# Optimization experiments

Hardware: AMD Instinct MI355X
Metric: run time of the kernel (lower is better)

Reference implementation:

```python
import jax, jax.numpy as jnp
import numpy as np

SCORE_THRESHOLD = 0.3
IOU_THRESHOLD = 0.5
TOP_K = 200
MAX_NMS_SIZE = 100
NEG = jnp.float32(-1e30)
NEG_HALF = jnp.float32(-1e29)


def _nms_per_class(scores, boxes):
    """Exact greedy NMS for one class. scores [N], boxes [N,4] (y1,x1,y2,x2).
    Returns (sel_scores [M], sel_boxes [M,4], valids [M]) with M=MAX_NMS_SIZE,
    zero-padded where fewer than M boxes survive (matches tf pad behavior)."""
    N = scores.shape[0]
    areas = jnp.prod(boxes[:, 2:] - boxes[:, :2], axis=-1)  # [N]
    arange_n = jnp.arange(N)
    # tf.image.non_max_suppression drops boxes with score < score_threshold
    masked0 = jnp.where(scores > SCORE_THRESHOLD, scores, NEG)

    def step(masked, _):
        idx = jnp.argmax(masked)
        s = masked[idx]
        valid = s > NEG_HALF
        box = boxes[idx]
        # IoU of selected box vs all boxes
        yx1 = jnp.maximum(box[:2], boxes[:, :2])
        yx2 = jnp.minimum(box[2:], boxes[:, 2:])
        inter = jnp.prod(jnp.maximum(yx2 - yx1, 0.0), axis=-1)
        union = jnp.prod(box[2:] - box[:2]) + areas - inter
        iou = jnp.where(union > 0, inter / union, 0.0)
        suppress = (iou > IOU_THRESHOLD) | (arange_n == idx)
        masked = jnp.where(valid & suppress, NEG, masked)
        return masked, (idx, valid, jnp.where(valid, s, 0.0))

    _, (idxs, valids, sel_scores) = jax.lax.scan(step, masked0, None, length=MAX_NMS_SIZE)
    sel_boxes = jnp.where(valids[:, None], boxes[idxs], 0.0)
    return sel_scores, sel_boxes, valids


def _per_sample(scores, boxes):
    """scores [N,C], boxes [N,4] -> (top_k_scores [K,2], top_k_boxes [K,4])."""
    cls_scores = scores[:, 1:].T  # [C-1, N]; class 0 (background) skipped
    sel_scores, sel_boxes, valids = jax.vmap(_nms_per_class, in_axes=(0, None))(cls_scores, boxes)
    ncls = cls_scores.shape[0]
    class_ids = jnp.where(valids, jnp.arange(1, ncls + 1, dtype=jnp.float32)[:, None], 0.0)
    flat_scores = jnp.stack([class_ids, sel_scores], axis=-1).reshape(-1, 2)  # [(C-1)*M, 2]
    flat_boxes = sel_boxes.reshape(-1, 4)
    n = flat_scores.shape[0]
    if TOP_K > n:  # static shapes -> Python-level pad branch
        flat_scores = jnp.pad(flat_scores, ((0, TOP_K - n), (0, 0)))
        flat_boxes = jnp.pad(flat_boxes, ((0, TOP_K - n), (0, 0)))
    _, top_idx = jax.lax.top_k(flat_scores[:, 1], TOP_K)
    return flat_scores[top_idx], flat_boxes[top_idx]


def setup_inputs() -> dict:
    key = jax.random.key(0)
    k1, k2, k3 = jax.random.split(key, 3)
    B, N, C = 16, 16384, 91
    scores_pred = jax.random.uniform(k1, (B, N, C), dtype=jnp.float32)
    tl = jax.random.uniform(k2, (B, N, 2), dtype=jnp.float32) * 0.8
    wh = jax.random.uniform(k3, (B, N, 2), dtype=jnp.float32) * 0.2 + 0.01
    boxes_pred = jnp.concatenate([tl, tl + wh], axis=-1)  # valid corner boxes
    return {"scores_pred": scores_pred, "boxes_pred": boxes_pred}


@jax.jit
def reference(scores_pred, boxes_pred):
    return jax.vmap(_per_sample)(scores_pred, boxes_pred)
```

## Files before the change

kernel.cpp:

```cpp
#include <hip/hip_runtime.h>

#define NTH 256
#define NBOX 16384
#define NCLSIN 91
#define NCLS 90
#define MAXSEL 100
#define TOPK 200
#define TSEL 256
#define CAP 1024
#define CANDL 512
#define CBCAP 256
#define BINS 1024
#define GRP 4
#define T0 0.989f
#define BOXPB 256
#define KSL 16
#define OVFC 64
#define CNTSTR 16

__device__ __forceinline__ unsigned fmap(float f) {
    unsigned u = __float_as_uint(f);
    return (u & 0x80000000u) ? ~u : (u | 0x80000000u);
}
__device__ __forceinline__ float funmap(unsigned u) {
    unsigned b = (u & 0x80000000u) ? (u ^ 0x80000000u) : ~u;
    return __uint_as_float(b);
}
__device__ __forceinline__ unsigned long long shfl_xor_u64(unsigned long long v, int mask) {
    unsigned lo = (unsigned)(v & 0xFFFFFFFFull);
    unsigned hi = (unsigned)(v >> 32);
    lo = __shfl_xor(lo, mask, 64);
    hi = __shfl_xor(hi, mask, 64);
    return ((unsigned long long)hi << 32) | (unsigned long long)lo;
}

__device__ __forceinline__ bool sup_test(float4 s, float sa, float4 c, float ca) {
    float y1 = fmaxf(s.x, c.x);
    float x1 = fmaxf(s.y, c.y);
    float y2 = fminf(s.z, c.z);
    float x2 = fminf(s.w, c.w);
    float dy = fmaxf(__fsub_rn(y2, y1), 0.f);
    float dx = fmaxf(__fsub_rn(x2, x1), 0.f);
    float inter = __fmul_rn(dy, dx);
    float uni = __fsub_rn(__fadd_rn(sa, ca), inter);
    if (!(uni > 0.f)) return false;
    float t = 0.5f * uni;
    if (inter <= t) return false;
    if (inter > __fmul_rn(t, 1.0000005f)) return true;
    return __fdiv_rn(inter, uni) > 0.5f;
}
__device__ __forceinline__ float box_area(float4 b) {
    return __fmul_rn(__fsub_rn(b.z, b.x), __fsub_rn(b.w, b.y));
}

__global__ __launch_bounds__(NTH) void zero_k(int4* __restrict__ p, int n4) {
    int i = blockIdx.x * NTH + threadIdx.x;
    if (i < n4) p[i] = make_int4(0, 0, 0, 0);
}

__device__ __forceinline__ void bin_select(unsigned* hist, unsigned* gbuf,
                                           int* sh_g, int* sh_b, unsigned* sh_pb,
                                           int tid, unsigned need) {
    unsigned gs = 0;
#pragma unroll
    for (int q = 0; q < GRP; ++q) gs += hist[tid * GRP + q];
    gbuf[tid] = gs;
    __syncthreads();
    for (int off = 1; off < NTH; off <<= 1) {
        unsigned add = (tid >= off) ? gbuf[tid - off] : 0u;
        __syncthreads();
        gbuf[tid] += add;
        __syncthreads();
    }
    if (tid == 0) *sh_g = NTH - 1;
    __syncthreads();
    if (gbuf[tid] >= need && (tid == 0 || gbuf[tid - 1] < need)) *sh_g = tid;
    __syncthreads();
    if (tid == 0) {
        int g = *sh_g;
        unsigned acc = (g > 0) ? gbuf[g - 1] : 0u;
        int bs = g * GRP + (GRP - 1);
        unsigned pb = acc;
#pragma unroll
        for (int q = 0; q < GRP; ++q) {
            acc += hist[g * GRP + q];
            if (acc >= need) { bs = g * GRP + q; pb = acc; break; }
            pb = acc;
        }
        *sh_b = bs; *sh_pb = pb;
    }
    __syncthreads();
}

__device__ __forceinline__ void sort_desc(unsigned long long* cand, int M, int tid) {
    int P = 1;
    while (P < M) P <<= 1;
    for (int i = M + tid; i < P; i += NTH) cand[i] = 0ull;
    __syncthreads();
    for (int kk = 2; kk <= P; kk <<= 1) {
        for (int jj = kk >> 1; jj > 0; jj >>= 1) {
            for (int i = tid; i < P; i += NTH) {
                int ixj = i ^ jj;
                if (ixj > i) {
                    unsigned long long a = cand[i], c = cand[ixj];
                    bool sw = ((i & kk) == 0) ? (a < c) : (a > c);
                    if (sw) { cand[i] = c; cand[ixj] = a; }
                }
            }
            __syncthreads();
        }
    }
}

__device__ __forceinline__ void emit_hit(unsigned long long pk, int b, int n0,
                                         int* cnt_s, unsigned long long* ent,
                                         unsigned* ovf_meta,
                                         unsigned long long* ovf_key,
                                         int* sh_ovf, int* cnt_g) {
    unsigned ee = (unsigned)pk;
    int row = (int)ee / NCLSIN;
    int c = (int)ee - row * NCLSIN;
    if (c == 0) return;
    unsigned i = (unsigned)(n0 + row);
    unsigned long long key = (pk & 0xFFFFFFFF00000000ull) | (0xFFFFFFFFu - i);
    int r = atomicAdd(&cnt_s[c], 1);
    if (r < KSL) {
        ent[c * KSL + r] = key;
    } else {
        int o = atomicAdd(sh_ovf, 1);
        if (o < OVFC) {
            ovf_meta[o] = ((unsigned)c << 16) | (unsigned)r;
            ovf_key[o] = key;
        } else {
            atomicAdd(&cnt_g[(b * NCLS + c - 1) * CNTSTR], CAP + 1);
        }
    }
}

__global__ __launch_bounds__(NTH) void filter_k(const float* __restrict__ in,
                                                unsigned long long* __restrict__ cand_g,
                                                int* __restrict__ cnt_g) {
    __shared__ int cnt_s[NCLSIN];
    __shared__ int base_s[NCLSIN];
    __shared__ unsigned long long ent[NCLSIN * KSL];
    __shared__ unsigned ovf_meta[OVFC];
    __shared__ unsigned long long ovf_key[OVFC];
    __shared__ int sh_ovf;

    const int tid = threadIdx.x;
    const int n0 = blockIdx.x * BOXPB;
    const int b = blockIdx.y;
    const int NF4 = BOXPB * NCLSIN / 4;

    for (int i = tid; i < NCLSIN; i += NTH) cnt_s[i] = 0;
    if (tid == 0) sh_ovf = 0;
    __syncthreads();

    unsigned long long q0 = 0, q1 = 0, q2 = 0, q3 = 0;
    int lc = 0;

    const float4* src = (const float4*)(in + ((size_t)b * NBOX + n0) * NCLSIN);
    for (int i = tid; i < NF4; i += 2 * NTH) {
        float4 v1 = src[i];
        int i2 = i + NTH;
        bool has2 = i2 < NF4;
        float4 v2 = make_float4(0.f, 0.f, 0.f, 0.f);
        if (has2) v2 = src[i2];
        float mx1 = fmaxf(fmaxf(v1.x, v1.y), fmaxf(v1.z, v1.w));
        float mx2 = fmaxf(fmaxf(v2.x, v2.y), fmaxf(v2.z, v2.w));
        if (fmaxf(mx1, mx2) > T0) {
#pragma unroll
            for (int h = 0; h < 2; ++h) {
                float4 v = h ? v2 : v1;
                float mx = h ? mx2 : mx1;
                int eb = (h ? i2 : i) * 4;
                if (mx > T0) {
                    const float sv[4] = {v.x, v.y, v.z, v.w};
#pragma unroll
                    for (int qq = 0; qq < 4; ++qq) {
                        float s = sv[qq];
                        if (s > T0) {
                            unsigned long long pk =
                                ((unsigned long long)fmap(s) << 32) |
                                (unsigned)(eb + qq);
                            if (lc == 0) q0 = pk;
                            else if (lc == 1) q1 = pk;
                            else if (lc == 2) q2 = pk;
                            else if (lc == 3) q3 = pk;
                            else emit_hit(pk, b, n0, cnt_s, ent, ovf_meta,
                                          ovf_key, &sh_ovf, cnt_g);
                            ++lc;
                        }
                    }
                }
            }
        }
    }
    if (lc > 0) emit_hit(q0, b, n0, cnt_s, ent, ovf_meta, ovf_key, &sh_ovf, cnt_g);
    if (lc > 1) emit_hit(q1, b, n0, cnt_s, ent, ovf_meta, ovf_key, &sh_ovf, cnt_g);
    if (lc > 2) emit_hit(q2, b, n0, cnt_s, ent, ovf_meta, ovf_key, &sh_ovf, cnt_g);
    if (lc > 3) emit_hit(q3, b, n0, cnt_s, ent, ovf_meta, ovf_key, &sh_ovf, cnt_g);
    __syncthreads();

    if (tid >= 1 && tid < NCLSIN) {
        int c = tid;
        int n = cnt_s[c];
        int base = 0;
        if (n > 0) {
            int bc = b * NCLS + c - 1;
            base = atomicAdd(&cnt_g[bc * CNTSTR], n);
            int lim = n < KSL ? n : KSL;
            for (int j = 0; j < lim; ++j) {
                int pos = base + j;
                if (pos < CAP) cand_g[(size_t)bc * CAP + pos] = ent[c * KSL + j];
            }
        }
        base_s[c] = base;
    }
    __syncthreads();

    int no = sh_ovf < OVFC ? sh_ovf : OVFC;
    for (int o = tid; o < no; o += NTH) {
        unsigned m = ovf_meta[o];
        int c = (int)(m >> 16);
        int r = (int)(m & 0xFFFFu);
        int bc = b * NCLS + c - 1;
        int pos = base_s[c] + r;
        if (pos < CAP) cand_g[(size_t)bc * CAP + pos] = ovf_key[o];
    }
}

__device__ __forceinline__ void serial_walk_lds(
    const unsigned long long* cand, int from, int to,
    const float4* __restrict__ bbase, const float4* candbox, const float* carea,
    float4* selbox, float* selarea, float* selscore,
    int& nsel, int* sh_nsel, int tid) {
    if (tid < 64) {
        for (int m = from; m < to && nsel < MAXSEL; ++m) {
            unsigned long long key = cand[m];
            float4 bx;
            float ca;
            if (m < CBCAP) { bx = candbox[m]; ca = carea[m]; }
            else { bx = bbase[(int)(0xFFFFFFFFu - (unsigned)key)]; ca = box_area(bx); }
            bool sup = false;
            if (tid < nsel) sup = sup_test(selbox[tid], selarea[tid], bx, ca);
            int l2 = tid + 64;
            if (l2 < nsel) sup = sup || sup_test(selbox[l2], selarea[l2], bx, ca);
            if (!__any(sup)) {
                if (tid == 0) {
                    selbox[nsel] = bx;
                    selarea[nsel] = ca;
                    selscore[nsel] = funmap((unsigned)(key >> 32));
                }
                nsel++;
            }
        }
        if (tid == 0) *sh_nsel = nsel;
    }
    __syncthreads();
    nsel = *sh_nsel;
    __syncthreads();
}

__global__ __launch_bounds__(NTH) void nms_k(
    const unsigned long long* __restrict__ cand_g,
    const int* __restrict__ cnt_g,
    const float* __restrict__ scores_raw,
    const float4* __restrict__ boxes,
    float* __restrict__ ws_sc, float* __restrict__ ws_bx, int use_band) {
    __shared__ unsigned long long cand[CANDL];
    __shared__ float4 candbox[CBCAP];
    __shared__ float carea[CBCAP];
    __shared__ float4 selbox[MAXSEL];
    __shared__ float selarea[MAXSEL];
    __shared__ float selscore[MAXSEL];
    __shared__ unsigned M32[CBCAP * 2];
    __shared__ unsigned gbuf[NTH];
    __shared__ unsigned sh_kmax, sh_pb;
    __shared__ int sh_E, sh_g, sh_b, sh_cnt, sh_nsel;
    unsigned* hist = (unsigned*)candbox;

    const int tid = threadIdx.x;
    const int c0 = blockIdx.x;
    const int b = blockIdx.y;
    const int bc = b * NCLS + c0;
    const float* sraw = scores_raw + (size_t)b * NBOX * NCLSIN + (c0 + 1);
    const float4* bbase = boxes + (size_t)b * NBOX;

    int nsel = 0;
    unsigned long long lastk = ~0ull;

    if (use_band) {
        const int C = cnt_g[bc * CNTSTR];
        if (C > 0 && C <= CANDL) {
            if (C <= 256) {
                unsigned long long v =
                    (tid < C) ? cand_g[(size_t)bc * CAP + tid] : 0ull;
#pragma unroll
                for (int kk = 2; kk <= 256; kk <<= 1) {
#pragma unroll
                    for (int jj = kk >> 1; jj > 0; jj >>= 1) {
                        unsigned long long o;
                        if (jj >= 64) {
                            cand[tid] = v;
                            __syncthreads();
                            o = cand[tid ^ jj];
                            __syncthreads();
                        } else {
                            o = shfl_xor_u64(v, jj);
                        }
                        bool lower = (tid & jj) == 0;
                        bool desc = (tid & kk) == 0;
                        v = (lower == desc) ? (v > o ? v : o) : (v < o ? v : o);
                    }
                }
                cand[tid] = v;
                __syncthreads();

                if (tid < C) {
                    float4 bx = bbase[(int)(0xFFFFFFFFu - (unsigned)cand[tid])];
                    candbox[tid] = bx;
                    carea[tid] = box_area(bx);
                }
                M32[tid] = 0;
                M32[tid + NTH] = 0;
                __syncthreads();

                const int nbatch = (C + 63) >> 6;
                for (int p = tid; p < nbatch * 2016; p += NTH) {
                    int bt = p / 2016;
                    int q = p - bt * 2016;
                    int i = (int)((1.0f + sqrtf(1.0f + 8.0f * (float)q)) * 0.5f);
                    while (i * (i - 1) / 2 > q) --i;
                    while ((i + 1) * i / 2 <= q) ++i;
                    int j = q - i * (i - 1) / 2;
                    int gm = bt * 64 + i, gj = bt * 64 + j;
                    if (gm < C) {
                        if (sup_test(candbox[gj], carea[gj], candbox[gm], carea[gm]))
                            atomicOr(&M32[gm * 2 + (j >> 5)], 1u << (j & 31));
                    }
                }
                __syncthreads();

                if (tid < 64) {
                    for (int bt = 0; bt < nbatch && nsel < MAXSEL; ++bt) {
                        int m = bt * 64 + tid;
                        bool active = m < C;
                        float4 bx = make_float4(0.f, 0.f, 0.f, 0.f);
                        float ca = 0.f;
                        unsigned long long key = 0ull;
                        unsigned long long myM = 0ull;
                        if (active) {
                            key = cand[m];
                            bx = candbox[m];
                            ca = carea[m];
                            myM = ((unsigned long long)M32[m * 2 + 1] << 32) |
                                  M32[m * 2];
                        }
                        bool supV = !active;
                        for (int j = 0; j < nsel; ++j) {
                            if (active)
                                supV = supV || sup_test(selbox[j], selarea[j], bx, ca);
                        }
                        unsigned long long selb = ~__ballot(supV);
                        unsigned long long U = __ballot(myM != 0ull) & selb;
                        while (U) {
                            int mm = __builtin_ctzll(U);
                            U &= U - 1ull;
                            unsigned long long Mm =
                                ((unsigned long long)M32[(bt * 64 + mm) * 2 + 1] << 32) |
                                M32[(bt * 64 + mm) * 2];
                            unsigned long long below =
                                (mm == 0) ? 0ull : ((1ull << mm) - 1ull);
                            if ((selb >> mm) & 1ull) {
                                if (Mm & selb & below) selb &= ~(1ull << mm);
                            }
                        }
                        int avail = MAXSEL - nsel;
                        int pop = __builtin_popcountll(selb);
                        while (pop > avail) {
                            selb &= ~(1ull << (63 - __builtin_clzll(selb)));
                            --pop;
                        }
                        if ((selb >> tid) & 1ull) {
                            unsigned long long below =
                                (tid == 0) ? 0ull : ((1ull << tid) - 1ull);
                            int pos = nsel + __builtin_popcountll(selb & below);
                            selbox[pos] = bx;
                            selarea[pos] = ca;
                            selscore[pos] = funmap((unsigned)(key >> 32));
                        }
                        nsel += pop;
                    }
                    if (tid == 0) sh_nsel = nsel;
                }
                __syncthreads();
                nsel = sh_nsel;
                __syncthreads();
            } else {
                for (int i = tid; i < C; i += NTH)
                    cand[i] = cand_g[(size_t)bc * CAP + i];
                sort_desc(cand, C, tid);
                const int PBX = C < CBCAP ? C : CBCAP;
                for (int i = tid; i < PBX; i += NTH) {
                    float4 bx = bbase[(int)(0xFFFFFFFFu - (unsigned)cand[i])];
                    candbox[i] = bx;
                    carea[i] = box_area(bx);
                }
                __syncthreads();
                serial_walk_lds(cand, 0, C, bbase, candbox, carea,
                                selbox, selarea, selscore, nsel, &sh_nsel, tid);
            }
            lastk = cand[C - 1];
        }
    }

    while (nsel < MAXSEL) {
        unsigned km = 0, ce = 0;
        for (int i = tid; i < NBOX; i += NTH) {
            float s = sraw[(size_t)i * NCLSIN];
            unsigned k = (s > 0.3f) ? fmap(s) : 0u;
            if (k) {
                unsigned long long key =
                    ((unsigned long long)k << 32) | (0xFFFFFFFFu - (unsigned)i);
                if (key < lastk) { ce++; km = km > k ? km : k; }
            }
        }
#pragma unroll
        for (int off = 32; off > 0; off >>= 1) {
            unsigned o = (unsigned)__shfl_xor((int)km, off, 64);
            km = km > o ? km : o;
            ce += (unsigned)__shfl_xor((int)ce, off, 64);
        }
        if ((tid & 63) == 0) { gbuf[tid >> 6] = km; gbuf[8 + (tid >> 6)] = ce; }
        __syncthreads();
        if (tid == 0) {
            unsigned m2 = 0, c2 = 0;
            for (int w = 0; w < NTH / 64; ++w) {
                m2 = m2 > gbuf[w] ? m2 : gbuf[w];
                c2 += gbuf[8 + w];
            }
            sh_kmax = m2; sh_E = (int)c2;
        }
        __syncthreads();
        const int E = sh_E;
        const unsigned kmax = sh_kmax;
        if (E == 0) break;

        unsigned thr = 1u;
        if (E > TSEL) {
            for (int shift = 8;; shift += 4) {
                for (int i = tid; i < BINS; i += NTH) hist[i] = 0u;
                __syncthreads();
                for (int i = tid; i < NBOX; i += NTH) {
                    float s = sraw[(size_t)i * NCLSIN];
                    unsigned k = (s > 0.3f) ? fmap(s) : 0u;
                    if (k) {
                        unsigned long long key =
                            ((unsigned long long)k << 32) | (0xFFFFFFFFu - (unsigned)i);
                        if (key < lastk) {
                            unsigned bin = (kmax - k) >> shift;
                            if (bin < BINS - 1) atomicAdd(&hist[bin], 1u);
                        }
                    }
                }
                __syncthreads();
                bin_select(hist, gbuf, &sh_g, &sh_b, &sh_pb, tid, (unsigned)TSEL);
                if (sh_b < BINS - 1) {
                    long long t = (long long)kmax - ((long long)(sh_b + 1) << shift) + 1;
                    thr = (t < 1) ? 1u : (unsigned)t;
                    break;
                }
            }
        }

        if (tid == 0) sh_cnt = 0;
        __syncthreads();
        for (int i = tid; i < NBOX; i += NTH) {
            float s = sraw[(size_t)i * NCLSIN];
            unsigned k = (s > 0.3f) ? fmap(s) : 0u;
            if (k >= thr) {
                unsigned long long key =
                    ((unsigned long long)k << 32) | (0xFFFFFFFFu - (unsigned)i);
                if (key < lastk) {
                    int pos = atomicAdd(&sh_cnt, 1);
                    if (pos < CANDL) cand[pos] = key;
                }
            }
        }
        __syncthreads();
        const int M = sh_cnt < CANDL ? sh_cnt : CANDL;

        sort_desc(cand, M, tid);
        const int PBX = M < CBCAP ? M : CBCAP;
        for (int i = tid; i < PBX; i += NTH) {
            float4 bx = bbase[(int)(0xFFFFFFFFu - (unsigned)cand[i])];
            candbox[i] = bx;
            carea[i] = box_area(bx);
        }
        __syncthreads();
        serial_walk_lds(cand, 0, M, bbase, candbox, carea,
                        selbox, selarea, selscore, nsel, &sh_nsel, tid);
        if (nsel >= MAXSEL || E <= M) break;
        lastk = cand[M - 1];
        __syncthreads();
    }

    if (tid < MAXSEL) {
        bool v = tid < nsel;
        ws_sc[(size_t)bc * MAXSEL + tid] = v ? selscore[tid] : 0.f;
        ((float4*)ws_bx)[(size_t)bc * MAXSEL + tid] =
            v ? selbox[tid] : make_float4(0.f, 0.f, 0.f, 0.f);
    }
}

__global__ __launch_bounds__(NTH) void topk_k(const float* __restrict__ ws_sc,
                                              const float* __restrict__ ws_bx,
                                              float* __restrict__ out_sc,
                                              float* __restrict__ out_bx) {
    __shared__ unsigned hist[BINS];
    __shared__ unsigned gbuf[NTH];
    __shared__ unsigned long long cand[CANDL];
    __shared__ unsigned sh_kmax, sh_pb;
    __shared__ int sh_E, sh_g, sh_b, sh_cnt;

    const int tid = threadIdx.x;
    const int b = blockIdx.x;
    const int NF = NCLS * MAXSEL;
    const float* sp = ws_sc + (size_t)b * NF;

    unsigned km = 0, ce = 0;
    for (int f = tid; f < NF; f += NTH) {
        unsigned k = __float_as_uint(sp[f]);
        if (k) { ce++; km = km > k ? km : k; }
    }
#pragma unroll
    for (int off = 32; off > 0; off >>= 1) {
        unsigned o = (unsigned)__shfl_xor((int)km, off, 64);
        km = km > o ? km : o;
        ce += (unsigned)__shfl_xor((int)ce, off, 64);
    }
    if ((tid & 63) == 0) { gbuf[tid >> 6] = km; gbuf[8 + (tid >> 6)] = ce; }
    __syncthreads();
    if (tid == 0) {
        unsigned m2 = 0, c2 = 0;
        for (int w = 0; w < NTH / 64; ++w) {
            m2 = m2 > gbuf[w] ? m2 : gbuf[w];
            c2 += gbuf[8 + w];
        }
        sh_kmax = m2; sh_E = (int)c2;
    }
    __syncthreads();
    const int E = sh_E;
    const unsigned kmax = sh_kmax;

    unsigned thr = 1u;
    if (E > TOPK) {
        for (int shift = 8;; shift += 4) {
            for (int i = tid; i < BINS; i += NTH) hist[i] = 0u;
            __syncthreads();
            for (int f = tid; f < NF; f += NTH) {
                unsigned k = __float_as_uint(sp[f]);
                if (k) {
                    unsigned bin = (kmax - k) >> shift;
                    if (bin < BINS - 1) atomicAdd(&hist[bin], 1u);
                }
            }
            __syncthreads();
            bin_select(hist, gbuf, &sh_g, &sh_b, &sh_pb, tid, (unsigned)TOPK);
            if (sh_b < BINS - 1) {
                long long t = (long long)kmax - ((long long)(sh_b + 1) << shift) + 1;
                thr = (t < 1) ? 1u : (unsigned)t;
                break;
            }
        }
    }

    if (tid == 0) sh_cnt = 0;
    __syncthreads();
    for (int f = tid; f < NF; f += NTH) {
        unsigned k = __float_as_uint(sp[f]);
        if (k >= thr) {
            int pos = atomicAdd(&sh_cnt, 1);
            if (pos < CANDL)
                cand[pos] = ((unsigned long long)k << 32) | (0xFFFFFFFFu - (unsigned)f);
        }
    }
    __syncthreads();
    int M = sh_cnt < CANDL ? sh_cnt : CANDL;

    if (M < TOPK) {
        int lim = M + TOPK;
        if (lim > NF) lim = NF;
        for (int f = tid; f < lim; f += NTH) {
            unsigned k = __float_as_uint(sp[f]);
            if (k == 0) {
                int pos = atomicAdd(&sh_cnt, 1);
                if (pos < CANDL)
                    cand[pos] = (unsigned long long)(0xFFFFFFFFu - (unsigned)f);
            }
        }
        __syncthreads();
        M = sh_cnt < CANDL ? sh_cnt : CANDL;
    }

    sort_desc(cand, M, tid);

    for (int k = tid; k < TOPK; k += NTH) {
        float cls = 0.f, s = 0.f;
        float4 bx = make_float4(0.f, 0.f, 0.f, 0.f);
        if (k < M) {
            unsigned long long key = cand[k];
            unsigned f = 0xFFFFFFFFu - (unsigned)key;
            s = __uint_as_float((unsigned)(key >> 32));
            cls = (s > 0.f) ? (float)(f / MAXSEL + 1) : 0.f;
            bx = *(const float4*)(ws_bx + ((size_t)b * NF + f) * 4);
        }
        out_sc[((size_t)b * TOPK + k) * 2 + 0] = cls;
        out_sc[((size_t)b * TOPK + k) * 2 + 1] = s;
        ((float4*)out_bx)[(size_t)b * TOPK + k] = bx;
    }
}

extern "C" void kernel_launch(void* const* d_in, const int* in_sizes, int n_in,
                              void* d_out, int out_size, void* d_ws, size_t ws_size,
                              hipStream_t stream) {
    const float* scores = (const float*)d_in[0];
    const float4* boxes = (const float4*)d_in[1];
    float* out = (float*)d_out;

    const int B = in_sizes[1] / (NBOX * 4);
    const int NBC = B * NCLS;

    size_t off_cand = ((size_t)NBC * CNTSTR * 4 + 15) & ~(size_t)15;
    size_t off_sc = off_cand + (size_t)NBC * CAP * 8;
    size_t off_bx = off_sc + (size_t)NBC * MAXSEL * 4;
    size_t need = off_bx + (size_t)NBC * MAXSEL * 16;

    char* ws = (char*)d_ws;
    bool use_band = ws_size >= need;

    int* cnt_g;
    unsigned long long* cand_g;
    float *ws_sc, *ws_bx;
    if (use_band) {
        cnt_g = (int*)ws;
        cand_g = (unsigned long long*)(ws + off_cand);
        ws_sc = (float*)(ws + off_sc);
        ws_bx = (float*)(ws + off_bx);
    } else {
        cnt_g = (int*)ws;
        cand_g = (unsigned long long*)ws;
        ws_sc = (float*)ws;
        ws_bx = ws_sc + (size_t)NBC * MAXSEL;
    }

    if (use_band) {
        int n4 = NBC * CNTSTR / 4;
        zero_k<<<(n4 + NTH - 1) / NTH, NTH, 0, stream>>>((int4*)cnt_g, n4);
        filter_k<<<dim3(NBOX / BOXPB, B), NTH, 0, stream>>>(scores, cand_g, cnt_g);
    }
    nms_k<<<dim3(NCLS, B), NTH, 0, stream>>>(cand_g, cnt_g, scores, boxes,
                                             ws_sc, ws_bx, use_band ? 1 : 0);
    topk_k<<<B, NTH, 0, stream>>>(ws_sc, ws_bx, out, out + (size_t)B * TOPK * 2);
}
```

Baseline: 106.0 us.

## Build full pairwise suppression bitmask and unroll score-filter loads by four

In the band NMS path, the suppression bitmask now covers every candidate pair up to 256, not just pairs inside each 64-candidate batch. Each batch checks earlier selections with bitwise ANDs against stored per-batch selection masks, which replaces the serial loop of IoU tests against already selected boxes. The cost is a larger shared-memory mask and more pairwise IoU work up front. The candidate-filter kernel also issues four float4 loads per iteration instead of two to raise memory-level parallelism.

After: 134.4 us. +26.8%, slower.

```diff
diff --git a/kernel.cpp b/kernel.cpp
--- a/kernel.cpp
+++ b/kernel.cpp
@@ -159,41 +159,45 @@
     unsigned long long q0 = 0, q1 = 0, q2 = 0, q3 = 0;
     int lc = 0;
 
+    auto proc = [&](float4 v, float mx, int idx4) {
+        if (mx > T0) {
+            const float sv[4] = {v.x, v.y, v.z, v.w};
+#pragma unroll
+            for (int qq = 0; qq < 4; ++qq) {
+                float s = sv[qq];
+                if (s > T0) {
+                    unsigned long long pk =
+                        ((unsigned long long)fmap(s) << 32) |
+                        (unsigned)(idx4 * 4 + qq);
+                    if (lc == 0) q0 = pk;
+                    else if (lc == 1) q1 = pk;
+                    else if (lc == 2) q2 = pk;
+                    else if (lc == 3) q3 = pk;
+                    else emit_hit(pk, b, n0, cnt_s, ent, ovf_meta,
+                                  ovf_key, &sh_ovf, cnt_g);
+                    ++lc;
+                }
+            }
+        }
+    };
+
+    const float4 z4 = make_float4(0.f, 0.f, 0.f, 0.f);
     const float4* src = (const float4*)(in + ((size_t)b * NBOX + n0) * NCLSIN);
-    for (int i = tid; i < NF4; i += 2 * NTH) {
+    for (int i = tid; i < NF4; i += 4 * NTH) {
+        int ib = i + NTH, ic = i + 2 * NTH, id = i + 3 * NTH;
         float4 v1 = src[i];
-        int i2 = i + NTH;
-        bool has2 = i2 < NF4;
-        float4 v2 = make_float4(0.f, 0.f, 0.f, 0.f);
-        if (has2) v2 = src[i2];
-        float mx1 = fmaxf(fmaxf(v1.x, v1.y), fmaxf(v1.z, v1.w));
-        float mx2 = fmaxf(fmaxf(v2.x, v2.y), fmaxf(v2.z, v2.w));
-        if (fmaxf(mx1, mx2) > T0) {
-#pragma unroll
-            for (int h = 0; h < 2; ++h) {
-                float4 v = h ? v2 : v1;
-                float mx = h ? mx2 : mx1;
-                int eb = (h ? i2 : i) * 4;
-                if (mx > T0) {
-                    const float sv[4] = {v.x, v.y, v.z, v.w};
-#pragma unroll
-                    for (int qq = 0; qq < 4; ++qq) {
-                        float s = sv[qq];
-                        if (s > T0) {
-                            unsigned long long pk =
-                                ((unsigned long long)fmap(s) << 32) |
-                                (unsigned)(eb + qq);
-                            if (lc == 0) q0 = pk;
-                            else if (lc == 1) q1 = pk;
-                            else if (lc == 2) q2 = pk;
-                            else if (lc == 3) q3 = pk;
-                            else emit_hit(pk, b, n0, cnt_s, ent, ovf_meta,
-                                          ovf_key, &sh_ovf, cnt_g);
-                            ++lc;
-                        }
-                    }
-                }
-            }
+        float4 v2 = (ib < NF4) ? src[ib] : z4;
+        float4 v3 = (ic < NF4) ? src[ic] : z4;
+        float4 v4 = (id < NF4) ? src[id] : z4;
+        float m1 = fmaxf(fmaxf(v1.x, v1.y), fmaxf(v1.z, v1.w));
+        float m2 = fmaxf(fmaxf(v2.x, v2.y), fmaxf(v2.z, v2.w));
+        float m3 = fmaxf(fmaxf(v3.x, v3.y), fmaxf(v3.z, v3.w));
+        float m4 = fmaxf(fmaxf(v4.x, v4.y), fmaxf(v4.z, v4.w));
+        if (fmaxf(fmaxf(m1, m2), fmaxf(m3, m4)) > T0) {
+            proc(v1, m1, i);
+            proc(v2, m2, ib);
+            proc(v3, m3, ic);
+            proc(v4, m4, id);
         }
     }
     if (lc > 0) emit_hit(q0, b, n0, cnt_s, ent, ovf_meta, ovf_key, &sh_ovf, cnt_g);
@@ -274,7 +278,7 @@
     __shared__ float4 selbox[MAXSEL];
     __shared__ float selarea[MAXSEL];
     __shared__ float selscore[MAXSEL];
-    __shared__ unsigned M32[CBCAP * 2];
+    __shared__ unsigned M32[CBCAP * 8];
     __shared__ unsigned gbuf[NTH];
     __shared__ unsigned sh_kmax, sh_pb;
     __shared__ int sh_E, sh_g, sh_b, sh_cnt, sh_nsel;
@@ -322,54 +326,56 @@
                     candbox[tid] = bx;
                     carea[tid] = box_area(bx);
                 }
-                M32[tid] = 0;
-                M32[tid + NTH] = 0;
-                __syncthreads();
-
-                const int nbatch = (C + 63) >> 6;
-                for (int p = tid; p < nbatch * 2016; p += NTH) {
-                    int bt = p / 2016;
-                    int q = p - bt * 2016;
-                    int i = (int)((1.0f + sqrtf(1.0f + 8.0f * (float)q)) * 0.5f);
-                    while (i * (i - 1) / 2 > q) --i;
-                    while ((i + 1) * i / 2 <= q) ++i;
-                    int j = q - i * (i - 1) / 2;
-                    int gm = bt * 64 + i, gj = bt * 64 + j;
-                    if (gm < C) {
-                        if (sup_test(candbox[gj], carea[gj], candbox[gm], carea[gm]))
-                            atomicOr(&M32[gm * 2 + (j >> 5)], 1u << (j & 31));
-                    }
+#pragma unroll
+                for (int w = 0; w < 8; ++w) M32[tid + w * NTH] = 0;
+                __syncthreads();
+
+                const int P2 = C * (C - 1) / 2;
+                for (int p = tid; p < P2; p += NTH) {
+                    int i = (int)((1.0f + sqrtf(1.0f + 8.0f * (float)p)) * 0.5f);
+                    while (i * (i - 1) / 2 > p) --i;
+                    while ((i + 1) * i / 2 <= p) ++i;
+                    int j = p - i * (i - 1) / 2;
+                    if (sup_test(candbox[j], carea[j], candbox[i], carea[i]))
+                        atomicOr(&M32[i * 8 + (j >> 5)], 1u << (j & 31));
                 }
                 __syncthreads();
 
                 if (tid < 64) {
+                    unsigned long long S0 = 0, S1 = 0, S2 = 0, S3 = 0;
+                    const int nbatch = (C + 63) >> 6;
                     for (int bt = 0; bt < nbatch && nsel < MAXSEL; ++bt) {
                         int m = bt * 64 + tid;
                         bool active = m < C;
                         float4 bx = make_float4(0.f, 0.f, 0.f, 0.f);
                         float ca = 0.f;
                         unsigned long long key = 0ull;
-                        unsigned long long myM = 0ull;
+                        unsigned long long w0 = 0, w1 = 0, w2 = 0, w3 = 0;
                         if (active) {
                             key = cand[m];
                             bx = candbox[m];
                             ca = carea[m];
-                            myM = ((unsigned long long)M32[m * 2 + 1] << 32) |
-                                  M32[m * 2];
+                            w0 = ((unsigned long long)M32[m * 8 + 1] << 32) | M32[m * 8 + 0];
+                            w1 = ((unsigned long long)M32[m * 8 + 3] << 32) | M32[m * 8 + 2];
+                            w2 = ((unsigned long long)M32[m * 8 + 5] << 32) | M32[m * 8 + 4];
+                            w3 = ((unsigned long long)M32[m * 8 + 7] << 32) | M32[m * 8 + 6];
                         }
-                        bool supV = !active;
-                        for (int j = 0; j < nsel; ++j) {
-                            if (active)
-                                supV = supV || sup_test(selbox[j], selarea[j], bx, ca);
-                        }
-                        unsigned long long selb = ~__ballot(supV);
-                        unsigned long long U = __ballot(myM != 0ull) & selb;
+                        unsigned long long myIntra =
+                            (bt == 0) ? w0 : (bt == 1) ? w1 : (bt == 2) ? w2 : w3;
+                        unsigned long long hitPrev = 0ull;
+                        if (bt > 0) hitPrev |= w0 & S0;
+                        if (bt > 1) hitPrev |= w1 & S1;
+                        if (bt > 2) hitPrev |= w2 & S2;
+                        bool dead = !active || (hitPrev != 0ull);
+                        unsigned long long selb = ~__ballot(dead);
+                        unsigned long long U = __ballot(active && myIntra != 0ull) & selb;
                         while (U) {
                             int mm = __builtin_ctzll(U);
                             U &= U - 1ull;
+                            int gm = bt * 64 + mm;
                             unsigned long long Mm =
-                                ((unsigned long long)M32[(bt * 64 + mm) * 2 + 1] << 32) |
-                                M32[(bt * 64 + mm) * 2];
+                                ((unsigned long long)M32[gm * 8 + bt * 2 + 1] << 32) |
+                                M32[gm * 8 + bt * 2];
                             unsigned long long below =
                                 (mm == 0) ? 0ull : ((1ull << mm) - 1ull);
                             if ((selb >> mm) & 1ull) {
@@ -390,6 +396,10 @@
                             selarea[pos] = ca;
                             selscore[pos] = funmap((unsigned)(key >> 32));
                         }
+                        if (bt == 0) S0 = selb;
+                        else if (bt == 1) S1 = selb;
+                        else if (bt == 2) S2 = selb;
+                        else S3 = selb;
                         nsel += pop;
                     }
                     if (tid == 0) sh_nsel = nsel;
```

## Replace global atomic candidate append with per-block fixed slots and drop zeroing kernel

Applied to the files above, without the earlier changes.

The filter kernel now writes each block's per-class hit count and up to KSL candidates into fixed slots indexed by block id, rather than using global atomics to append into a compacted list. This removes the zero_k launch and the overflow path. The NMS kernel builds a prefix sum over the 64 per-block counts and compacts the candidates itself, falling back when any block overflows KSL. The filter loop is also unrolled from two to four float4 loads per iteration. The cost moves to the NMS kernel, which now reads 64 counts and a sparse 1024-slot region per class.

Measured after the change: 104.8 us. Within noise of the previous version (-1.1%).

```diff
diff --git a/kernel.cpp b/kernel.cpp
--- a/kernel.cpp
+++ b/kernel.cpp
@@ -10,12 +10,12 @@
 #define CAP 1024
 #define CANDL 512
 #define CBCAP 256
+#define NBLK 64
 #define BINS 1024
 #define GRP 4
 #define T0 0.989f
 #define BOXPB 256
 #define KSL 16
-#define OVFC 64
 #define CNTSTR 16
 
 __device__ __forceinline__ unsigned fmap(float f) {
@@ -53,11 +53,6 @@
     return __fmul_rn(__fsub_rn(b.z, b.x), __fsub_rn(b.w, b.y));
 }
 
-__global__ __launch_bounds__(NTH) void zero_k(int4* __restrict__ p, int n4) {
-    int i = blockIdx.x * NTH + threadIdx.x;
-    if (i < n4) p[i] = make_int4(0, 0, 0, 0);
-}
-
 __device__ __forceinline__ void bin_select(unsigned* hist, unsigned* gbuf,
                                            int* sh_g, int* sh_b, unsigned* sh_pb,
                                            int tid, unsigned need) {
@@ -112,121 +107,88 @@
     }
 }
 
-__device__ __forceinline__ void emit_hit(unsigned long long pk, int b, int n0,
-                                         int* cnt_s, unsigned long long* ent,
-                                         unsigned* ovf_meta,
-                                         unsigned long long* ovf_key,
-                                         int* sh_ovf, int* cnt_g) {
-    unsigned ee = (unsigned)pk;
-    int row = (int)ee / NCLSIN;
-    int c = (int)ee - row * NCLSIN;
-    if (c == 0) return;
-    unsigned i = (unsigned)(n0 + row);
-    unsigned long long key = (pk & 0xFFFFFFFF00000000ull) | (0xFFFFFFFFu - i);
-    int r = atomicAdd(&cnt_s[c], 1);
-    if (r < KSL) {
-        ent[c * KSL + r] = key;
-    } else {
-        int o = atomicAdd(sh_ovf, 1);
-        if (o < OVFC) {
-            ovf_meta[o] = ((unsigned)c << 16) | (unsigned)r;
-            ovf_key[o] = key;
-        } else {
-            atomicAdd(&cnt_g[(b * NCLS + c - 1) * CNTSTR], CAP + 1);
-        }
-    }
-}
-
 __global__ __launch_bounds__(NTH) void filter_k(const float* __restrict__ in,
                                                 unsigned long long* __restrict__ cand_g,
-                                                int* __restrict__ cnt_g) {
+                                                int* __restrict__ cnt2) {
     __shared__ int cnt_s[NCLSIN];
-    __shared__ int base_s[NCLSIN];
     __shared__ unsigned long long ent[NCLSIN * KSL];
-    __shared__ unsigned ovf_meta[OVFC];
-    __shared__ unsigned long long ovf_key[OVFC];
-    __shared__ int sh_ovf;
 
     const int tid = threadIdx.x;
-    const int n0 = blockIdx.x * BOXPB;
+    const int blkid = blockIdx.x;
+    const int n0 = blkid * BOXPB;
     const int b = blockIdx.y;
     const int NF4 = BOXPB * NCLSIN / 4;
 
     for (int i = tid; i < NCLSIN; i += NTH) cnt_s[i] = 0;
-    if (tid == 0) sh_ovf = 0;
     __syncthreads();
 
     unsigned long long q0 = 0, q1 = 0, q2 = 0, q3 = 0;
     int lc = 0;
 
+    auto emit = [&](unsigned long long pk) {
+        unsigned ee = (unsigned)pk;
+        int row = (int)ee / NCLSIN;
+        int c = (int)ee - row * NCLSIN;
+        if (c == 0) return;
+        unsigned i = (unsigned)(n0 + row);
+        unsigned long long key = (pk & 0xFFFFFFFF00000000ull) | (0xFFFFFFFFu - i);
+        int r = atomicAdd(&cnt_s[c], 1);
+        if (r < KSL) ent[c * KSL + r] = key;
+    };
+    auto proc = [&](float4 v, float mx, int idx4) {
+        if (mx > T0) {
+            const float sv[4] = {v.x, v.y, v.z, v.w};
+#pragma unroll
+            for (int qq = 0; qq < 4; ++qq) {
+                float s = sv[qq];
+                if (s > T0) {
+                    unsigned long long pk =
+                        ((unsigned long long)fmap(s) << 32) |
+                        (unsigned)(idx4 * 4 + qq);
+                    if (lc == 0) q0 = pk;
+                    else if (lc == 1) q1 = pk;
+                    else if (lc == 2) q2 = pk;
+                    else if (lc == 3) q3 = pk;
+                    else emit(pk);
+                    ++lc;
+                }
+            }
+        }
+    };
+
+    const float4 z4 = make_float4(0.f, 0.f, 0.f, 0.f);
     const float4* src = (const float4*)(in + ((size_t)b * NBOX + n0) * NCLSIN);
-    for (int i = tid; i < NF4; i += 2 * NTH) {
+    for (int i = tid; i < NF4; i += 4 * NTH) {
+        int ib = i + NTH, ic = i + 2 * NTH, id = i + 3 * NTH;
         float4 v1 = src[i];
-        int i2 = i + NTH;
-        bool has2 = i2 < NF4;
-        float4 v2 = make_float4(0.f, 0.f, 0.f, 0.f);
-        if (has2) v2 = src[i2];
-        float mx1 = fmaxf(fmaxf(v1.x, v1.y), fmaxf(v1.z, v1.w));
-        float mx2 = fmaxf(fmaxf(v2.x, v2.y), fmaxf(v2.z, v2.w));
-        if (fmaxf(mx1, mx2) > T0) {
-#pragma unroll
-            for (int h = 0; h < 2; ++h) {
-                float4 v = h ? v2 : v1;
-                float mx = h ? mx2 : mx1;
-                int eb = (h ? i2 : i) * 4;
-                if (mx > T0) {
-                    const float sv[4] = {v.x, v.y, v.z, v.w};
-#pragma unroll
-                    for (int qq = 0; qq < 4; ++qq) {
-                        float s = sv[qq];
-                        if (s > T0) {
-                            unsigned long long pk =
-                                ((unsigned long long)fmap(s) << 32) |
-                                (unsigned)(eb + qq);
-                            if (lc == 0) q0 = pk;
-                            else if (lc == 1) q1 = pk;
-                            else if (lc == 2) q2 = pk;
-                            else if (lc == 3) q3 = pk;
-                            else emit_hit(pk, b, n0, cnt_s, ent, ovf_meta,
-                                          ovf_key, &sh_ovf, cnt_g);
-                            ++lc;
-                        }
-                    }
-                }
-            }
-        }
-    }
-    if (lc > 0) emit_hit(q0, b, n0, cnt_s, ent, ovf_meta, ovf_key, &sh_ovf, cnt_g);
-    if (lc > 1) emit_hit(q1, b, n0, cnt_s, ent, ovf_meta, ovf_key, &sh_ovf, cnt_g);
-    if (lc > 2) emit_hit(q2, b, n0, cnt_s, ent, ovf_meta, ovf_key, &sh_ovf, cnt_g);
-    if (lc > 3) emit_hit(q3, b, n0, cnt_s, ent, ovf_meta, ovf_key, &sh_ovf, cnt_g);
+        float4 v2 = (ib < NF4) ? src[ib] : z4;
+        float4 v3 = (ic < NF4) ? src[ic] : z4;
+        float4 v4 = (id < NF4) ? src[id] : z4;
+        float m1 = fmaxf(fmaxf(v1.x, v1.y), fmaxf(v1.z, v1.w));
+        float m2 = fmaxf(fmaxf(v2.x, v2.y), fmaxf(v2.z, v2.w));
+        float m3 = fmaxf(fmaxf(v3.x, v3.y), fmaxf(v3.z, v3.w));
+        float m4 = fmaxf(fmaxf(v4.x, v4.y), fmaxf(v4.z, v4.w));
+        if (fmaxf(fmaxf(m1, m2), fmaxf(m3, m4)) > T0) {
+            proc(v1, m1, i);
+            proc(v2, m2, ib);
+            proc(v3, m3, ic);
+            proc(v4, m4, id);
+        }
+    }
+    if (lc > 0) emit(q0);
+    if (lc > 1) emit(q1);
+    if (lc > 2) emit(q2);
+    if (lc > 3) emit(q3);
     __syncthreads();
 
     if (tid >= 1 && tid < NCLSIN) {
         int c = tid;
         int n = cnt_s[c];
-        int base = 0;
-        if (n > 0) {
-            int bc = b * NCLS + c - 1;
-            base = atomicAdd(&cnt_g[bc * CNTSTR], n);
-            int lim = n < KSL ? n : KSL;
-            for (int j = 0; j < lim; ++j) {
-                int pos = base + j;
-                if (pos < CAP) cand_g[(size_t)bc * CAP + pos] = ent[c * KSL + j];
-            }
-        }
-        base_s[c] = base;
-    }
-    __syncthreads();
-
-    int no = sh_ovf < OVFC ? sh_ovf : OVFC;
-    for (int o = tid; o < no; o += NTH) {
-        unsigned m = ovf_meta[o];
-        int c = (int)(m >> 16);
-        int r = (int)(m & 0xFFFFu);
         int bc = b * NCLS + c - 1;
-        int pos = base_s[c] + r;
-        if (pos < CAP) cand_g[(size_t)bc * CAP + pos] = ovf_key[o];
+        cnt2[(size_t)bc * NBLK + blkid] = n;
+        int lim = n < KSL ? n : KSL;
+        for (int j = 0; j < lim; ++j)
+            cand_g[(size_t)bc * CAP + blkid * KSL + j] = ent[c * KSL + j];
     }
 }
 
@@ -264,7 +226,7 @@
 
 __global__ __launch_bounds__(NTH) void nms_k(
     const unsigned long long* __restrict__ cand_g,
-    const int* __restrict__ cnt_g,
+    const int* __restrict__ cnt2,
     const float* __restrict__ scores_raw,
     const float4* __restrict__ boxes,
     float* __restrict__ ws_sc, float* __restrict__ ws_bx, int use_band) {
@@ -275,9 +237,11 @@
     __shared__ float selarea[MAXSEL];
     __shared__ float selscore[MAXSEL];
     __shared__ unsigned M32[CBCAP * 2];
+    __shared__ int scnt[NBLK];
+    __shared__ int spref[NBLK];
     __shared__ unsigned gbuf[NTH];
     __shared__ unsigned sh_kmax, sh_pb;
-    __shared__ int sh_E, sh_g, sh_b, sh_cnt, sh_nsel;
+    __shared__ int sh_E, sh_g, sh_b, sh_cnt, sh_nsel, sh_C;
     unsigned* hist = (unsigned*)candbox;
 
     const int tid = threadIdx.x;
@@ -290,12 +254,35 @@
     int nsel = 0;
     unsigned long long lastk = ~0ull;
 
+    int C = 0;
     if (use_band) {
-        const int C = cnt_g[bc * CNTSTR];
+        if (tid < NBLK) scnt[tid] = cnt2[(size_t)bc * NBLK + tid];
+        __syncthreads();
+        if (tid == 0) {
+            int acc = 0;
+            bool bad = false;
+            for (int k2 = 0; k2 < NBLK; ++k2) {
+                spref[k2] = acc;
+                int n = scnt[k2];
+                if (n > KSL) bad = true;
+                acc += n;
+            }
+            sh_C = bad ? -1 : acc;
+        }
+        __syncthreads();
+        C = sh_C;
         if (C > 0 && C <= CANDL) {
+            for (int idx = tid; idx < NBLK * KSL; idx += NTH) {
+                int blk = idx >> 4, r = idx & (KSL - 1);
+                if (r < scnt[blk])
+                    cand[spref[blk] + r] =
+                        cand_g[(size_t)bc * CAP + blk * KSL + r];
+            }
+            __syncthreads();
+
             if (C <= 256) {
-                unsigned long long v =
-                    (tid < C) ? cand_g[(size_t)bc * CAP + tid] : 0ull;
+                unsigned long long v = (tid < C) ? cand[tid] : 0ull;
+                __syncthreads();
 #pragma unroll
                 for (int kk = 2; kk <= 256; kk <<= 1) {
 #pragma unroll
@@ -398,8 +385,6 @@
                 nsel = sh_nsel;
                 __syncthreads();
             } else {
-                for (int i = tid; i < C; i += NTH)
-                    cand[i] = cand_g[(size_t)bc * CAP + i];
                 sort_desc(cand, C, tid);
                 const int PBX = C < CBCAP ? C : CBCAP;
                 for (int i = tid; i < PBX; i += NTH) {
@@ -632,7 +617,7 @@
     const int B = in_sizes[1] / (NBOX * 4);
     const int NBC = B * NCLS;
 
-    size_t off_cand = ((size_t)NBC * CNTSTR * 4 + 15) & ~(size_t)15;
+    size_t off_cand = ((size_t)NBC * NBLK * 4 + 15) & ~(size_t)15;
     size_t off_sc = off_cand + (size_t)NBC * CAP * 8;
     size_t off_bx = off_sc + (size_t)NBC * MAXSEL * 4;
     size_t need = off_bx + (size_t)NBC * MAXSEL * 16;
@@ -640,27 +625,25 @@
     char* ws = (char*)d_ws;
     bool use_band = ws_size >= need;
 
-    int* cnt_g;
+    int* cnt2;
     unsigned long long* cand_g;
     float *ws_sc, *ws_bx;
     if (use_band) {
-        cnt_g = (int*)ws;
+        cnt2 = (int*)ws;
         cand_g = (unsigned long long*)(ws + off_cand);
         ws_sc = (float*)(ws + off_sc);
         ws_bx = (float*)(ws + off_bx);
     } else {
-        cnt_g = (int*)ws;
+        cnt2 = (int*)ws;
         cand_g = (unsigned long long*)ws;
         ws_sc = (float*)ws;
         ws_bx = ws_sc + (size_t)NBC * MAXSEL;
     }
 
     if (use_band) {
-        int n4 = NBC * CNTSTR / 4;
-        zero_k<<<(n4 + NTH - 1) / NTH, NTH, 0, stream>>>((int4*)cnt_g, n4);
-        filter_k<<<dim3(NBOX / BOXPB, B), NTH, 0, stream>>>(scores, cand_g, cnt_g);
-    }
-    nms_k<<<dim3(NCLS, B), NTH, 0, stream>>>(cand_g, cnt_g, scores, boxes,
+        filter_k<<<dim3(NBOX / BOXPB, B), NTH, 0, stream>>>(scores, cand_g, cnt2);
+    }
+    nms_k<<<dim3(NCLS, B), NTH, 0, stream>>>(cand_g, cnt2, scores, boxes,
                                              ws_sc, ws_bx, use_band ? 1 : 0);
     topk_k<<<B, NTH, 0, stream>>>(ws_sc, ws_bx, out, out + (size_t)B * TOPK * 2);
 }
```
